# Performance work log

Measured on AMD Instinct MI355X. Metric: run time of the kernel, lower is better.

## Reference

```python
import jax, jax.numpy as jnp
import numpy as np

N_NODES = 100000
N_EDGES = 1600000
D_IN, D_HID, D_OUT = 256, 512, 48
K_STEPS = 10
ALPHA = 0.1


def setup_inputs() -> dict:
    key = jax.random.key(0)
    k_x, k_e, k_w1, k_w2 = jax.random.split(key, 4)
    x = jax.random.normal(k_x, (N_NODES, D_IN), dtype=jnp.float32)
    edge_index = jax.random.randint(k_e, (2, N_EDGES), 0, N_NODES, dtype=jnp.int64)
    # MLP params (Kaiming-ish scaling)
    W1 = jax.random.normal(k_w1, (D_IN, D_HID), dtype=jnp.float32) * (1.0 / np.sqrt(D_IN))
    b1 = jnp.zeros((D_HID,), dtype=jnp.float32)
    W2 = jax.random.normal(k_w2, (D_HID, D_OUT), dtype=jnp.float32) * (1.0 / np.sqrt(D_HID))
    b2 = jnp.zeros((D_OUT,), dtype=jnp.float32)
    return {"x": x, "edge_index": edge_index, "W1": W1, "b1": b1, "W2": W2, "b2": b2}


def reference(x, edge_index, W1, b1, W2, b2):
    N = x.shape[0]
    # --- MLP encoder ---
    h = jax.nn.relu(x @ W1 + b1) @ W2 + b2  # [N, D_OUT]

    # --- APPNP propagation (PyG defaults: add self-loops, symmetric gcn_norm) ---
    loop = jnp.arange(N, dtype=edge_index.dtype)
    src = jnp.concatenate([edge_index[0], loop])  # [E+N]
    dst = jnp.concatenate([edge_index[1], loop])
    ones = jnp.ones(src.shape[0], dtype=h.dtype)
    deg = jax.ops.segment_sum(ones, dst, num_segments=N)  # in-degree incl. self-loop
    dinv = jnp.where(deg > 0, jax.lax.rsqrt(deg), 0.0)
    norm = dinv[src] * dinv[dst]  # [E+N]

    out = h
    for _ in range(K_STEPS):
        msg = out[src] * norm[:, None]                      # gather + scale
        agg = jax.ops.segment_sum(msg, dst, num_segments=N)  # scatter-add
        out = (1.0 - ALPHA) * agg + ALPHA * h                # teleport mix
    return out
```

## Files before the change

### kernel.cpp

```cpp
#include <hip/hip_runtime.h>
#include <hip/hip_fp16.h>

constexpr int D_IN = 256, D_HID = 512, D_OUT = 48;
constexpr int HPAD = 64;
constexpr int K_STEPS = 10;

typedef __attribute__((ext_vector_type(8))) __bf16 bf16x8;
typedef __attribute__((ext_vector_type(4))) float f32x4;

__device__ __forceinline__ unsigned short f2bf(float f) {
  unsigned u = __builtin_bit_cast(unsigned, f);
  u += 0x7fffu + ((u >> 16) & 1u);
  return (unsigned short)(u >> 16);
}

__device__ __forceinline__ void gl2lds16(const unsigned short* g, unsigned short* l) {
  __builtin_amdgcn_global_load_lds(
      (const __attribute__((address_space(1))) unsigned int*)g,
      (__attribute__((address_space(3))) unsigned int*)l, 16, 0, 0);
}


__global__ void zero1_kernel(int* __restrict__ a, int N) {
  int i = blockIdx.x * 256 + threadIdx.x;
  if (i < N) a[i] = 0;
}

__global__ __launch_bounds__(256) void count_kernel(const int* __restrict__ dst,
                                                    int* __restrict__ cnt,
                                                    int* __restrict__ rank, int E) {
  int e = blockIdx.x * 256 + threadIdx.x;
  if (e >= E) return;
  int d = __builtin_nontemporal_load(dst + e);
  int r = atomicAdd(&cnt[d], 1);
  __builtin_nontemporal_store(r, rank + e);
}

__global__ void dinv_kernel(const int* __restrict__ cnt, float* __restrict__ dinv, int N) {
  int n = blockIdx.x * 256 + threadIdx.x;
  if (n < N) dinv[n] = rsqrtf((float)(cnt[n] + 1));
}

__global__ void scan1_kernel(const int* __restrict__ cnt, int* __restrict__ row_ptr,
                             int* __restrict__ bsum, int N) {
  __shared__ int sd[256];
  int tid = threadIdx.x, b = blockIdx.x;
  int i0 = b * 1024 + tid * 4;
  int v[4];
#pragma unroll
  for (int m = 0; m < 4; ++m) v[m] = (i0 + m < N) ? ((cnt[i0 + m] + 4) & ~3) : 0;
  int s = v[0] + v[1] + v[2] + v[3];
  sd[tid] = s;
  __syncthreads();
  for (int off = 1; off < 256; off <<= 1) {
    int t = (tid >= off) ? sd[tid - off] : 0;
    __syncthreads();
    sd[tid] += t;
    __syncthreads();
  }
  int run = sd[tid] - s;
#pragma unroll
  for (int m = 0; m < 4; ++m) {
    if (i0 + m < N) row_ptr[i0 + m] = run;
    run += v[m];
  }
  if (tid == 255) bsum[b] = sd[255];
}

__global__ void scan2_kernel(const int* __restrict__ bsum, int* __restrict__ bofs,
                             int* __restrict__ row_ptr, int NB, int N) {
  __shared__ int sd[128];
  int tid = threadIdx.x;
  int v = (tid < NB) ? bsum[tid] : 0;
  sd[tid] = v;
  __syncthreads();
  for (int off = 1; off < 128; off <<= 1) {
    int t = (tid >= off) ? sd[tid - off] : 0;
    __syncthreads();
    sd[tid] += t;
    __syncthreads();
  }
  if (tid < NB) bofs[tid] = sd[tid] - v;
  if (tid == 127) row_ptr[N] = sd[127];
}

__global__ void scan3_kernel(int* __restrict__ row_ptr, const int* __restrict__ bofs, int N) {
  int b = blockIdx.x;
  if (b == 0) return;
  int add = bofs[b];
  int i0 = b * 1024 + threadIdx.x * 4;
#pragma unroll
  for (int m = 0; m < 4; ++m)
    if (i0 + m < N) row_ptr[i0 + m] += add;
}

__global__ __launch_bounds__(256) void fill_kernel(
    const int* __restrict__ src, const int* __restrict__ dst,
    const int* __restrict__ row_ptr, const int* __restrict__ rank,
    int* __restrict__ edges, int E) {
  int e = blockIdx.x * 256 + threadIdx.x;
  if (e >= E) return;
  int d = __builtin_nontemporal_load(dst + e);
  int s = __builtin_nontemporal_load(src + e);
  int r = __builtin_nontemporal_load(rank + e);
  edges[row_ptr[d] + r] = s;
}

__global__ void pad_kernel(const int* __restrict__ cnt, const int* __restrict__ row_ptr,
                           int* __restrict__ edges, int N) {
  int n = blockIdx.x * 256 + threadIdx.x;
  if (n >= N) return;
  int a = row_ptr[n] + cnt[n];
  int b = row_ptr[n + 1];
  edges[a] = n;
  for (int p = a + 1; p < b; ++p) edges[p] = N;
}

__global__ void zrow_kernel(__half* __restrict__ a, __half* __restrict__ b, int N) {
  int t = threadIdx.x;
  a[(size_t)N * HPAD + t] = __float2half(0.f);
  b[(size_t)N * HPAD + t] = __float2half(0.f);
}


__global__ void convert_w1(const float* __restrict__ W1, unsigned short* __restrict__ W1F) {
  int i = blockIdx.x * 256 + threadIdx.x;
  if (i >= D_HID * D_IN) return;
  int c = i >> 8, k = i & 255;
  int ct = c >> 6, tn = (c >> 4) & 3, l15 = c & 15;
  int kb = k >> 5, q = (k >> 3) & 3, j = k & 7;
  int lane = (q << 4) | l15;
  int dst = (((ct * 4 + tn) * 8 + kb) << 9) + lane * 8 + j;
  W1F[dst] = f2bf(W1[k * D_HID + c]);
}

__global__ void convert_w2(const float* __restrict__ W2, unsigned short* __restrict__ W2F) {
  int i = blockIdx.x * 256 + threadIdx.x;
  if (i >= D_OUT * D_HID) return;
  int n = i >> 9, k = i & 511;
  int ct = k >> 6, kk = (k >> 5) & 1, q = (k >> 3) & 3, j = k & 7;
  int tn = n >> 4, l15 = n & 15;
  int lane = (q << 4) | l15;
  int dst = (((ct * 2 + kk) * 3 + tn) << 9) + lane * 8 + j;
  W2F[dst] = f2bf(W2[k * D_OUT + n]);
}


__global__ __launch_bounds__(512, 4) void encoder_kernel(
    const float* __restrict__ x, const float* __restrict__ b1,
    const float* __restrict__ b2, const float* __restrict__ dinvp,
    const unsigned short* __restrict__ W1F,
    const unsigned short* __restrict__ W2F,
    __half* __restrict__ h2, __half* __restrict__ qb, int N) {
  __shared__ unsigned short sW1[16384];
  __shared__ unsigned short sHid[8][16][72];
  __shared__ float sB1[512];
  __shared__ float sB2[64];

  int tid = threadIdx.x;
  int w = tid >> 6, lane = tid & 63;
  int q = lane >> 4, l15 = lane & 15;
  int row0 = blockIdx.x * 128 + w * 16;

  {
    const unsigned short* gsrc = W1F + (w << 9) + lane * 8;
    unsigned short* ldst = &sW1[w << 9];
#pragma unroll
    for (int i = 0; i < 4; ++i)
      gl2lds16(gsrc + (i << 12), ldst + (i << 12));
  }
  sB1[tid] = b1[tid];
  if (tid < 48) sB2[tid] = b2[tid];

  int grow = row0 + l15;
  bool rok = grow < N;
  const float* xr = x + (size_t)grow * D_IN;
  float4 xv[16];
#pragma unroll
  for (int jb = 0; jb < 8; ++jb) {
    xv[2 * jb]     = rok ? *(const float4*)(xr + jb * 32 + q * 8)
                         : make_float4(0.f, 0.f, 0.f, 0.f);
    xv[2 * jb + 1] = rok ? *(const float4*)(xr + jb * 32 + q * 8 + 4)
                         : make_float4(0.f, 0.f, 0.f, 0.f);
  }
  uint4 axu[8];
#pragma unroll
  for (int jb = 0; jb < 8; ++jb) {
    union { uint4 u; unsigned short s[8]; } uu;
    float4 v0 = xv[2 * jb], v1 = xv[2 * jb + 1];
    uu.s[0] = f2bf(v0.x); uu.s[1] = f2bf(v0.y); uu.s[2] = f2bf(v0.z); uu.s[3] = f2bf(v0.w);
    uu.s[4] = f2bf(v1.x); uu.s[5] = f2bf(v1.y); uu.s[6] = f2bf(v1.z); uu.s[7] = f2bf(v1.w);
    axu[jb] = uu.u;
  }

  f32x4 hacc[3];
#pragma unroll
  for (int t = 0; t < 3; ++t)
#pragma unroll
    for (int r = 0; r < 4; ++r) hacc[t][r] = 0.f;

  __syncthreads();

  for (int ct = 0; ct < 8; ++ct) {
    int c0 = ct * 64;
    f32x4 acc[4];
#pragma unroll
    for (int t = 0; t < 4; ++t)
#pragma unroll
      for (int r = 0; r < 4; ++r) acc[t][r] = 0.f;

    const unsigned short* sb = &sW1[lane * 8];
#pragma unroll
    for (int kb = 0; kb < 8; ++kb) {
      bf16x8 a = __builtin_bit_cast(bf16x8, axu[kb]);
      bf16x8 bq0 = *(const bf16x8*)(sb + (kb << 9));
      bf16x8 bq1 = *(const bf16x8*)(sb + (kb << 9) + 4096);
      bf16x8 bq2 = *(const bf16x8*)(sb + (kb << 9) + 8192);
      bf16x8 bq3 = *(const bf16x8*)(sb + (kb << 9) + 12288);
      acc[0] = __builtin_amdgcn_mfma_f32_16x16x32_bf16(a, bq0, acc[0], 0, 0, 0);
      acc[1] = __builtin_amdgcn_mfma_f32_16x16x32_bf16(a, bq1, acc[1], 0, 0, 0);
      acc[2] = __builtin_amdgcn_mfma_f32_16x16x32_bf16(a, bq2, acc[2], 0, 0, 0);
      acc[3] = __builtin_amdgcn_mfma_f32_16x16x32_bf16(a, bq3, acc[3], 0, 0, 0);
    }
#pragma unroll
    for (int tn = 0; tn < 4; ++tn) {
      int c = tn * 16 + l15;
      float bias = sB1[c0 + c];
#pragma unroll
      for (int rg = 0; rg < 4; ++rg) {
        float v = acc[tn][rg] + bias;
        v = v > 0.f ? v : 0.f;
        sHid[w][q * 4 + rg][c] = f2bf(v);
      }
    }
#pragma unroll
    for (int kk = 0; kk < 2; ++kk) {
      bf16x8 a0 = *(const bf16x8*)&sHid[w][l15][kk * 32 + q * 8];
      const unsigned short* w2b = W2F + (((ct * 2 + kk) * 3) << 9) + lane * 8;
#pragma unroll
      for (int tn = 0; tn < 3; ++tn) {
        bf16x8 b = *(const bf16x8*)(w2b + (tn << 9));
        hacc[tn] = __builtin_amdgcn_mfma_f32_16x16x32_bf16(a0, b, hacc[tn], 0, 0, 0);
      }
    }
    __syncthreads();
    if (ct < 7) {
      const unsigned short* gsrc = W1F + ((size_t)(ct + 1) << 14) + (w << 9) + lane * 8;
      unsigned short* ldst = &sW1[w << 9];
#pragma unroll
      for (int i = 0; i < 4; ++i)
        gl2lds16(gsrc + (i << 12), ldst + (i << 12));
      __syncthreads();
    }
  }
  float dv[4];
#pragma unroll
  for (int rg = 0; rg < 4; ++rg) {
    int gr = row0 + q * 4 + rg;
    dv[rg] = (gr < N) ? dinvp[gr] : 0.f;
  }
#pragma unroll
  for (int tn = 0; tn < 3; ++tn) {
    int c = tn * 16 + l15;
    float bias = sB2[c];
#pragma unroll
    for (int rg = 0; rg < 4; ++rg) {
      int gr = row0 + q * 4 + rg;
      if (gr < N) {
        float val = hacc[tn][rg] + bias;
        h2[(size_t)gr * HPAD + c] = __float2half(val);
        qb[(size_t)gr * HPAD + c] = __float2half(dv[rg] * val);
      }
    }
  }
#pragma unroll
  for (int rg = 0; rg < 4; ++rg) {
    int gr = row0 + q * 4 + rg;
    if (gr < N) {
      h2[(size_t)gr * HPAD + 48 + l15] = __float2half(0.f);
      qb[(size_t)gr * HPAD + 48 + l15] = __float2half(0.f);
    }
  }
}


__global__ __launch_bounds__(256) void prop_kernel(
    const __half* __restrict__ cur, const __half* __restrict__ h2,
    const float* __restrict__ dinv, const int* __restrict__ row_ptr,
    const int* __restrict__ edges, __half* __restrict__ nxt,
    float* __restrict__ outf, int N, int last) {
  int wid = (blockIdx.x * 256 + threadIdx.x) >> 6;
  int lane = threadIdx.x & 63;
  int half = lane >> 5;
  int slot = (lane >> 3) & 3;
  int s = lane & 7;
  int node = wid * 2 + half;
  bool nok = node < N;
  int p0 = 0, p1 = 0;
  if (nok) { int2 pp = *(const int2*)(row_ptr + node); p0 = pp.x; p1 = pp.y; }
  int d = p1 - p0;
  int dmax = max(d, __shfl_xor(d, 32));
  int nb = dmax >> 2;

  float acc[8];
#pragma unroll
  for (int i = 0; i < 8; ++i) acc[i] = 0.f;

  int p = p0 + slot;
  int e0 = N, e1 = N;
  if (nb > 0) e0 = edges[p];
  if (nb > 1) e1 = edges[p + 4];
  int b = 0;
  for (; b + 2 <= nb; b += 2) {
    int n0 = N, n1 = N;
    if (b + 2 < nb) n0 = edges[p + 8];
    if (b + 3 < nb) n1 = edges[p + 12];
    int i0 = (p < p1) ? e0 : N;
    int i1 = (p + 4 < p1) ? e1 : N;
    union { float4 f; __half2 h[4]; } u0, u1;
    u0.f = *(const float4*)(cur + ((size_t)i0 << 6) + s * 8);
    u1.f = *(const float4*)(cur + ((size_t)i1 << 6) + s * 8);
#pragma unroll
    for (int i = 0; i < 4; ++i) {
      float2 f0 = __half22float2(u0.h[i]);
      float2 f1 = __half22float2(u1.h[i]);
      acc[2 * i]     += f0.x + f1.x;
      acc[2 * i + 1] += f0.y + f1.y;
    }
    e0 = n0; e1 = n1; p += 8;
  }
  if (b < nb) {
    int i0 = (p < p1) ? e0 : N;
    union { float4 f; __half2 h[4]; } u0;
    u0.f = *(const float4*)(cur + ((size_t)i0 << 6) + s * 8);
#pragma unroll
    for (int i = 0; i < 4; ++i) {
      float2 f0 = __half22float2(u0.h[i]);
      acc[2 * i]     += f0.x;
      acc[2 * i + 1] += f0.y;
    }
  }
#pragma unroll
  for (int i = 0; i < 8; ++i) {
    acc[i] += __int_as_float(__builtin_amdgcn_ds_swizzle(__float_as_int(acc[i]), 0x201F));
    acc[i] += __int_as_float(__builtin_amdgcn_ds_swizzle(__float_as_int(acc[i]), 0x401F));
  }
  if ((lane & 24) != 0 || !nok) return;
  float di = dinv[node];
  size_t base = ((size_t)node << 6) + s * 8;
  union { float4 f; __half2 h[4]; } uh;
  uh.f = *(const float4*)(h2 + base);
  float outv[8];
#pragma unroll
  for (int i = 0; i < 4; ++i) {
    float2 hf = __half22float2(uh.h[i]);
    outv[2 * i]     = 0.9f * di * acc[2 * i]     + 0.1f * hf.x;
    outv[2 * i + 1] = 0.9f * di * acc[2 * i + 1] + 0.1f * hf.y;
  }
  if (last) {
    if (s < 6) {
      float* op = outf + (size_t)node * D_OUT + s * 8;
      *(float4*)op       = make_float4(outv[0], outv[1], outv[2], outv[3]);
      *(float4*)(op + 4) = make_float4(outv[4], outv[5], outv[6], outv[7]);
    }
  } else {
    union { uint4 u4; __half2 h[4]; } o;
#pragma unroll
    for (int i = 0; i < 4; ++i)
      o.h[i] = __floats2half2_rn(di * outv[2 * i], di * outv[2 * i + 1]);
    *(uint4*)(nxt + base) = o.u4;
  }
}


extern "C" void kernel_launch(void* const* d_in, const int* in_sizes, int n_in,
                              void* d_out, int out_size, void* d_ws, size_t ws_size,
                              hipStream_t stream) {
  (void)n_in; (void)out_size; (void)ws_size;
  const float* x  = (const float*)d_in[0];
  const int*   ei = (const int*)d_in[1];
  const float* W1 = (const float*)d_in[2];
  const float* b1 = (const float*)d_in[3];
  const float* W2 = (const float*)d_in[4];
  const float* b2 = (const float*)d_in[5];
  const int N = in_sizes[0] / D_IN;
  const int E = in_sizes[1] / 2;
  const int* e_src = ei;
  const int* e_dst = ei + E;

  char* ws = (char*)d_ws;
  size_t off = 0;
  auto take = [&](size_t bytes) -> char* {
    char* p = ws + off;
    off += (bytes + 511) & ~(size_t)511;
    return p;
  };
  int* cnt      = (int*)take((size_t)N * 4);
  float* dinv   = (float*)take((size_t)N * 4);
  int* row_ptr  = (int*)take((size_t)(N + 1) * 4);
  int* bsum     = (int*)take(1024);
  int* bofs     = (int*)take(1024);
  int* rank     = (int*)take((size_t)E * 4);
  int* edges    = (int*)take(((size_t)E + 4 * (size_t)N + 1024) * 4);
  unsigned short* W1F = (unsigned short*)take((size_t)D_IN * D_HID * 2);
  unsigned short* W2F = (unsigned short*)take((size_t)D_HID * D_OUT * 2);
  __half* h2    = (__half*)take((size_t)N * HPAD * 2);
  __half* bufA  = (__half*)take((size_t)(N + 1) * HPAD * 2);
  __half* bufB  = (__half*)d_out;
  float* outp   = (float*)d_out;

  int nb256 = (N + 255) / 256;
  int eb256 = (E + 255) / 256;
  int NB    = (N + 1023) / 1024;

  zero1_kernel<<<nb256, 256, 0, stream>>>(cnt, N);
  count_kernel<<<eb256, 256, 0, stream>>>(e_dst, cnt, rank, E);
  dinv_kernel<<<nb256, 256, 0, stream>>>(cnt, dinv, N);
  scan1_kernel<<<NB, 256, 0, stream>>>(cnt, row_ptr, bsum, N);
  scan2_kernel<<<1, 128, 0, stream>>>(bsum, bofs, row_ptr, NB, N);
  scan3_kernel<<<NB, 256, 0, stream>>>(row_ptr, bofs, N);
  fill_kernel<<<eb256, 256, 0, stream>>>(e_src, e_dst, row_ptr, rank, edges, E);
  pad_kernel<<<nb256, 256, 0, stream>>>(cnt, row_ptr, edges, N);
  zrow_kernel<<<1, 64, 0, stream>>>(bufA, bufB, N);

  convert_w1<<<(D_IN * D_HID + 255) / 256, 256, 0, stream>>>(W1, W1F);
  convert_w2<<<(D_HID * D_OUT + 255) / 256, 256, 0, stream>>>(W2, W2F);
  encoder_kernel<<<(N + 127) / 128, 512, 0, stream>>>(x, b1, b2, dinv, W1F, W2F,
                                                      h2, bufB, N);

  int waves = (N + 1) / 2;
  int pblocks = (waves + 3) / 4;
  const __half* src = bufB;
  __half* dst = bufA;
  for (int it = 1; it <= K_STEPS; ++it) {
    int last = (it == K_STEPS);
    prop_kernel<<<pblocks, 256, 0, stream>>>(src, h2, dinv, row_ptr, edges,
                                             dst, outp, N, last);
    src = dst;
    dst = (dst == bufA) ? bufB : bufA;
  }
}
```

Baseline: 668.9 us.

## Make encoder persistent with x prefetch overlap; unroll propagation gather by four

The encoder becomes a persistent kernel of 256 blocks that loop over 128-row strips. The next strip's x rows are prefetched into registers inside the W1-chunk loop so global loads overlap the MFMA work, and launch bounds drop to 2 waves per SIMD. Separately, the propagation kernel's neighbor gather is unrolled from 2 to 4 edge loads per iteration, with tail handling, to raise memory-level parallelism. The risks are higher register pressure and lower occupancy in the encoder, and only 256 blocks may underfill the GPU.

```diff
diff --git a/kernel.cpp b/kernel.cpp
--- a/kernel.cpp
+++ b/kernel.cpp
@@ -146,7 +146,7 @@
 }
 
 
-__global__ __launch_bounds__(512, 4) void encoder_kernel(
+__global__ __launch_bounds__(512, 2) void encoder_kernel(
     const float* __restrict__ x, const float* __restrict__ b1,
     const float* __restrict__ b2, const float* __restrict__ dinvp,
     const unsigned short* __restrict__ W1F,
@@ -160,126 +160,147 @@
   int tid = threadIdx.x;
   int w = tid >> 6, lane = tid & 63;
   int q = lane >> 4, l15 = lane & 15;
-  int row0 = blockIdx.x * 128 + w * 16;
-
-  {
-    const unsigned short* gsrc = W1F + (w << 9) + lane * 8;
+  const int nStrips = (N + 127) >> 7;
+
+  auto stageCt = [&](int c) {
+    const unsigned short* gsrc = W1F + ((size_t)c << 14) + (w << 9) + lane * 8;
     unsigned short* ldst = &sW1[w << 9];
 #pragma unroll
     for (int i = 0; i < 4; ++i)
       gl2lds16(gsrc + (i << 12), ldst + (i << 12));
-  }
+  };
+
+  int strip = blockIdx.x;
+  stageCt(0);
   sB1[tid] = b1[tid];
   if (tid < 48) sB2[tid] = b2[tid];
 
-  int grow = row0 + l15;
-  bool rok = grow < N;
-  const float* xr = x + (size_t)grow * D_IN;
   float4 xv[16];
-#pragma unroll
-  for (int jb = 0; jb < 8; ++jb) {
-    xv[2 * jb]     = rok ? *(const float4*)(xr + jb * 32 + q * 8)
-                         : make_float4(0.f, 0.f, 0.f, 0.f);
-    xv[2 * jb + 1] = rok ? *(const float4*)(xr + jb * 32 + q * 8 + 4)
-                         : make_float4(0.f, 0.f, 0.f, 0.f);
-  }
-  uint4 axu[8];
-#pragma unroll
-  for (int jb = 0; jb < 8; ++jb) {
-    union { uint4 u; unsigned short s[8]; } uu;
-    float4 v0 = xv[2 * jb], v1 = xv[2 * jb + 1];
-    uu.s[0] = f2bf(v0.x); uu.s[1] = f2bf(v0.y); uu.s[2] = f2bf(v0.z); uu.s[3] = f2bf(v0.w);
-    uu.s[4] = f2bf(v1.x); uu.s[5] = f2bf(v1.y); uu.s[6] = f2bf(v1.z); uu.s[7] = f2bf(v1.w);
-    axu[jb] = uu.u;
-  }
-
-  f32x4 hacc[3];
-#pragma unroll
-  for (int t = 0; t < 3; ++t)
-#pragma unroll
-    for (int r = 0; r < 4; ++r) hacc[t][r] = 0.f;
-
+  {
+    int grow = strip * 128 + w * 16 + l15;
+    bool rok = grow < N;
+    const float* xr = x + (size_t)grow * D_IN;
+#pragma unroll
+    for (int jb = 0; jb < 8; ++jb) {
+      xv[2 * jb]     = rok ? *(const float4*)(xr + jb * 32 + q * 8)
+                           : make_float4(0.f, 0.f, 0.f, 0.f);
+      xv[2 * jb + 1] = rok ? *(const float4*)(xr + jb * 32 + q * 8 + 4)
+                           : make_float4(0.f, 0.f, 0.f, 0.f);
+    }
+  }
   __syncthreads();
 
-  for (int ct = 0; ct < 8; ++ct) {
-    int c0 = ct * 64;
-    f32x4 acc[4];
-#pragma unroll
-    for (int t = 0; t < 4; ++t)
-#pragma unroll
-      for (int r = 0; r < 4; ++r) acc[t][r] = 0.f;
-
-    const unsigned short* sb = &sW1[lane * 8];
-#pragma unroll
-    for (int kb = 0; kb < 8; ++kb) {
-      bf16x8 a = __builtin_bit_cast(bf16x8, axu[kb]);
-      bf16x8 bq0 = *(const bf16x8*)(sb + (kb << 9));
-      bf16x8 bq1 = *(const bf16x8*)(sb + (kb << 9) + 4096);
-      bf16x8 bq2 = *(const bf16x8*)(sb + (kb << 9) + 8192);
-      bf16x8 bq3 = *(const bf16x8*)(sb + (kb << 9) + 12288);
-      acc[0] = __builtin_amdgcn_mfma_f32_16x16x32_bf16(a, bq0, acc[0], 0, 0, 0);
-      acc[1] = __builtin_amdgcn_mfma_f32_16x16x32_bf16(a, bq1, acc[1], 0, 0, 0);
-      acc[2] = __builtin_amdgcn_mfma_f32_16x16x32_bf16(a, bq2, acc[2], 0, 0, 0);
-      acc[3] = __builtin_amdgcn_mfma_f32_16x16x32_bf16(a, bq3, acc[3], 0, 0, 0);
-    }
-#pragma unroll
-    for (int tn = 0; tn < 4; ++tn) {
+  for (;;) {
+    int nxt = strip + 256;
+    bool hasNext = nxt < nStrips;
+    int ngrow = nxt * 128 + w * 16 + l15;
+    bool nok = hasNext && (ngrow < N);
+    const float* nxr = x + (size_t)ngrow * D_IN;
+
+    uint4 axu[8];
+#pragma unroll
+    for (int jb = 0; jb < 8; ++jb) {
+      union { uint4 u; unsigned short s[8]; } uu;
+      float4 v0 = xv[2 * jb], v1 = xv[2 * jb + 1];
+      uu.s[0] = f2bf(v0.x); uu.s[1] = f2bf(v0.y); uu.s[2] = f2bf(v0.z); uu.s[3] = f2bf(v0.w);
+      uu.s[4] = f2bf(v1.x); uu.s[5] = f2bf(v1.y); uu.s[6] = f2bf(v1.z); uu.s[7] = f2bf(v1.w);
+      axu[jb] = uu.u;
+    }
+
+    f32x4 hacc[3];
+#pragma unroll
+    for (int t = 0; t < 3; ++t)
+#pragma unroll
+      for (int r = 0; r < 4; ++r) hacc[t][r] = 0.f;
+
+#pragma unroll
+    for (int ct = 0; ct < 8; ++ct) {
+      int c0 = ct * 64;
+      f32x4 acc[4];
+#pragma unroll
+      for (int t = 0; t < 4; ++t)
+#pragma unroll
+        for (int r = 0; r < 4; ++r) acc[t][r] = 0.f;
+
+      const unsigned short* sb = &sW1[lane * 8];
+#pragma unroll
+      for (int kb = 0; kb < 8; ++kb) {
+        bf16x8 a = __builtin_bit_cast(bf16x8, axu[kb]);
+        bf16x8 bq0 = *(const bf16x8*)(sb + (kb << 9));
+        bf16x8 bq1 = *(const bf16x8*)(sb + (kb << 9) + 4096);
+        bf16x8 bq2 = *(const bf16x8*)(sb + (kb << 9) + 8192);
+        bf16x8 bq3 = *(const bf16x8*)(sb + (kb << 9) + 12288);
+        acc[0] = __builtin_amdgcn_mfma_f32_16x16x32_bf16(a, bq0, acc[0], 0, 0, 0);
+        acc[1] = __builtin_amdgcn_mfma_f32_16x16x32_bf16(a, bq1, acc[1], 0, 0, 0);
+        acc[2] = __builtin_amdgcn_mfma_f32_16x16x32_bf16(a, bq2, acc[2], 0, 0, 0);
+        acc[3] = __builtin_amdgcn_mfma_f32_16x16x32_bf16(a, bq3, acc[3], 0, 0, 0);
+      }
+#pragma unroll
+      for (int tn = 0; tn < 4; ++tn) {
+        int c = tn * 16 + l15;
+        float bias = sB1[c0 + c];
+#pragma unroll
+        for (int rg = 0; rg < 4; ++rg) {
+          float v = acc[tn][rg] + bias;
+          v = v > 0.f ? v : 0.f;
+          sHid[w][q * 4 + rg][c] = f2bf(v);
+        }
+      }
+#pragma unroll
+      for (int kk = 0; kk < 2; ++kk) {
+        bf16x8 a0 = *(const bf16x8*)&sHid[w][l15][kk * 32 + q * 8];
+        const unsigned short* w2b = W2F + (((ct * 2 + kk) * 3) << 9) + lane * 8;
+#pragma unroll
+        for (int tn = 0; tn < 3; ++tn) {
+          bf16x8 b = *(const bf16x8*)(w2b + (tn << 9));
+          hacc[tn] = __builtin_amdgcn_mfma_f32_16x16x32_bf16(a0, b, hacc[tn], 0, 0, 0);
+        }
+      }
+      __syncthreads();
+      if (ct < 7) stageCt(ct + 1);
+      if (hasNext) {
+        xv[2 * ct]     = nok ? *(const float4*)(nxr + ct * 32 + q * 8)
+                             : make_float4(0.f, 0.f, 0.f, 0.f);
+        xv[2 * ct + 1] = nok ? *(const float4*)(nxr + ct * 32 + q * 8 + 4)
+                             : make_float4(0.f, 0.f, 0.f, 0.f);
+      }
+      __syncthreads();
+    }
+
+    int row0 = strip * 128 + w * 16;
+    float dv[4];
+#pragma unroll
+    for (int rg = 0; rg < 4; ++rg) {
+      int gr = row0 + q * 4 + rg;
+      dv[rg] = (gr < N) ? dinvp[gr] : 0.f;
+    }
+#pragma unroll
+    for (int tn = 0; tn < 3; ++tn) {
       int c = tn * 16 + l15;
-      float bias = sB1[c0 + c];
+      float bias = sB2[c];
 #pragma unroll
       for (int rg = 0; rg < 4; ++rg) {
-        float v = acc[tn][rg] + bias;
-        v = v > 0.f ? v : 0.f;
-        sHid[w][q * 4 + rg][c] = f2bf(v);
-      }
-    }
-#pragma unroll
-    for (int kk = 0; kk < 2; ++kk) {
-      bf16x8 a0 = *(const bf16x8*)&sHid[w][l15][kk * 32 + q * 8];
-      const unsigned short* w2b = W2F + (((ct * 2 + kk) * 3) << 9) + lane * 8;
-#pragma unroll
-      for (int tn = 0; tn < 3; ++tn) {
-        bf16x8 b = *(const bf16x8*)(w2b + (tn << 9));
-        hacc[tn] = __builtin_amdgcn_mfma_f32_16x16x32_bf16(a0, b, hacc[tn], 0, 0, 0);
-      }
-    }
-    __syncthreads();
-    if (ct < 7) {
-      const unsigned short* gsrc = W1F + ((size_t)(ct + 1) << 14) + (w << 9) + lane * 8;
-      unsigned short* ldst = &sW1[w << 9];
-#pragma unroll
-      for (int i = 0; i < 4; ++i)
-        gl2lds16(gsrc + (i << 12), ldst + (i << 12));
-      __syncthreads();
-    }
-  }
-  float dv[4];
-#pragma unroll
-  for (int rg = 0; rg < 4; ++rg) {
-    int gr = row0 + q * 4 + rg;
-    dv[rg] = (gr < N) ? dinvp[gr] : 0.f;
-  }
-#pragma unroll
-  for (int tn = 0; tn < 3; ++tn) {
-    int c = tn * 16 + l15;
-    float bias = sB2[c];
+        int gr = row0 + q * 4 + rg;
+        if (gr < N) {
+          float val = hacc[tn][rg] + bias;
+          h2[(size_t)gr * HPAD + c] = __float2half(val);
+          qb[(size_t)gr * HPAD + c] = __float2half(dv[rg] * val);
+        }
+      }
+    }
 #pragma unroll
     for (int rg = 0; rg < 4; ++rg) {
       int gr = row0 + q * 4 + rg;
       if (gr < N) {
-        float val = hacc[tn][rg] + bias;
-        h2[(size_t)gr * HPAD + c] = __float2half(val);
-        qb[(size_t)gr * HPAD + c] = __float2half(dv[rg] * val);
-      }
-    }
-  }
-#pragma unroll
-  for (int rg = 0; rg < 4; ++rg) {
-    int gr = row0 + q * 4 + rg;
-    if (gr < N) {
-      h2[(size_t)gr * HPAD + 48 + l15] = __float2half(0.f);
-      qb[(size_t)gr * HPAD + 48 + l15] = __float2half(0.f);
-    }
+        h2[(size_t)gr * HPAD + 48 + l15] = __float2half(0.f);
+        qb[(size_t)gr * HPAD + 48 + l15] = __float2half(0.f);
+      }
+    }
+
+    if (!hasNext) break;
+    strip = nxt;
+    stageCt(0);
+    __syncthreads();
   }
 }
 
@@ -307,27 +328,37 @@
   for (int i = 0; i < 8; ++i) acc[i] = 0.f;
 
   int p = p0 + slot;
-  int e0 = N, e1 = N;
+  int e0 = N, e1 = N, e2 = N, e3 = N;
   if (nb > 0) e0 = edges[p];
   if (nb > 1) e1 = edges[p + 4];
+  if (nb > 2) e2 = edges[p + 8];
+  if (nb > 3) e3 = edges[p + 12];
   int b = 0;
-  for (; b + 2 <= nb; b += 2) {
-    int n0 = N, n1 = N;
-    if (b + 2 < nb) n0 = edges[p + 8];
-    if (b + 3 < nb) n1 = edges[p + 12];
-    int i0 = (p < p1) ? e0 : N;
-    int i1 = (p + 4 < p1) ? e1 : N;
-    union { float4 f; __half2 h[4]; } u0, u1;
+  for (; b + 4 <= nb; b += 4) {
+    int n0 = N, n1 = N, n2 = N, n3 = N;
+    if (b + 4 < nb) n0 = edges[p + 16];
+    if (b + 5 < nb) n1 = edges[p + 20];
+    if (b + 6 < nb) n2 = edges[p + 24];
+    if (b + 7 < nb) n3 = edges[p + 28];
+    int i0 = (p      < p1) ? e0 : N;
+    int i1 = (p + 4  < p1) ? e1 : N;
+    int i2 = (p + 8  < p1) ? e2 : N;
+    int i3 = (p + 12 < p1) ? e3 : N;
+    union { float4 f; __half2 h[4]; } u0, u1, u2, u3;
     u0.f = *(const float4*)(cur + ((size_t)i0 << 6) + s * 8);
     u1.f = *(const float4*)(cur + ((size_t)i1 << 6) + s * 8);
+    u2.f = *(const float4*)(cur + ((size_t)i2 << 6) + s * 8);
+    u3.f = *(const float4*)(cur + ((size_t)i3 << 6) + s * 8);
 #pragma unroll
     for (int i = 0; i < 4; ++i) {
       float2 f0 = __half22float2(u0.h[i]);
       float2 f1 = __half22float2(u1.h[i]);
-      acc[2 * i]     += f0.x + f1.x;
-      acc[2 * i + 1] += f0.y + f1.y;
-    }
-    e0 = n0; e1 = n1; p += 8;
+      float2 f2 = __half22float2(u2.h[i]);
+      float2 f3 = __half22float2(u3.h[i]);
+      acc[2 * i]     += (f0.x + f1.x) + (f2.x + f3.x);
+      acc[2 * i + 1] += (f0.y + f1.y) + (f2.y + f3.y);
+    }
+    e0 = n0; e1 = n1; e2 = n2; e3 = n3; p += 16;
   }
   if (b < nb) {
     int i0 = (p < p1) ? e0 : N;
@@ -338,6 +369,28 @@
       float2 f0 = __half22float2(u0.h[i]);
       acc[2 * i]     += f0.x;
       acc[2 * i + 1] += f0.y;
+    }
+  }
+  if (b + 1 < nb) {
+    int i1 = (p + 4 < p1) ? e1 : N;
+    union { float4 f; __half2 h[4]; } u1;
+    u1.f = *(const float4*)(cur + ((size_t)i1 << 6) + s * 8);
+#pragma unroll
+    for (int i = 0; i < 4; ++i) {
+      float2 f1 = __half22float2(u1.h[i]);
+      acc[2 * i]     += f1.x;
+      acc[2 * i + 1] += f1.y;
+    }
+  }
+  if (b + 2 < nb) {
+    int i2 = (p + 8 < p1) ? e2 : N;
+    union { float4 f; __half2 h[4]; } u2;
+    u2.f = *(const float4*)(cur + ((size_t)i2 << 6) + s * 8);
+#pragma unroll
+    for (int i = 0; i < 4; ++i) {
+      float2 f2 = __half22float2(u2.h[i]);
+      acc[2 * i]     += f2.x;
+      acc[2 * i + 1] += f2.y;
     }
   }
 #pragma unroll
@@ -425,8 +478,7 @@
 
   convert_w1<<<(D_IN * D_HID + 255) / 256, 256, 0, stream>>>(W1, W1F);
   convert_w2<<<(D_HID * D_OUT + 255) / 256, 256, 0, stream>>>(W2, W2F);
-  encoder_kernel<<<(N + 127) / 128, 512, 0, stream>>>(x, b1, b2, dinv, W1F, W2F,
-                                                      h2, bufB, N);
+  encoder_kernel<<<256, 512, 0, stream>>>(x, b1, b2, dinv, W1F, W2F, h2, bufB, N);
 
   int waves = (N + 1) / 2;
   int pblocks = (waves + 3) / 4;
```

After: 732.1 us. +9.4%, slower.

## Assign one wavefront per node with 8 edge slots and software-pipelined gathers

Applied to the files above, without the earlier changes.

The propagation kernel now gives each destination node a full 64-lane wavefront, with 8 edge slots of 8 lanes, instead of two nodes per wave with 4 slots each. CSR rows are padded to multiples of 8 to match, and the gather loop is rewritten with a 4-deep index prefetch and a one-ahead row load. The aim is more memory-level parallelism per node and removal of the divergent max-degree loop shared between half-waves. In exchange, rows carry more padding edges (reads of the zero row), and the wave count doubles, so more lanes sit idle for low-degree nodes.

```diff
diff --git a/kernel.cpp b/kernel.cpp
--- a/kernel.cpp
+++ b/kernel.cpp
@@ -48,7 +48,7 @@
   int i0 = b * 1024 + tid * 4;
   int v[4];
 #pragma unroll
-  for (int m = 0; m < 4; ++m) v[m] = (i0 + m < N) ? ((cnt[i0 + m] + 4) & ~3) : 0;
+  for (int m = 0; m < 4; ++m) v[m] = (i0 + m < N) ? ((cnt[i0 + m] + 8) & ~7) : 0;
   int s = v[0] + v[1] + v[2] + v[3];
   sd[tid] = s;
   __syncthreads();
@@ -291,61 +291,50 @@
     float* __restrict__ outf, int N, int last) {
   int wid = (blockIdx.x * 256 + threadIdx.x) >> 6;
   int lane = threadIdx.x & 63;
-  int half = lane >> 5;
-  int slot = (lane >> 3) & 3;
+  int slot = lane >> 3;
   int s = lane & 7;
-  int node = wid * 2 + half;
-  bool nok = node < N;
-  int p0 = 0, p1 = 0;
-  if (nok) { int2 pp = *(const int2*)(row_ptr + node); p0 = pp.x; p1 = pp.y; }
-  int d = p1 - p0;
-  int dmax = max(d, __shfl_xor(d, 32));
-  int nb = dmax >> 2;
+  int node = wid;
+  if (node >= N) return;
+  int2 pp = *(const int2*)(row_ptr + node);
+  int p = pp.x + slot;
+  int nb = (pp.y - pp.x) >> 3;
 
   float acc[8];
 #pragma unroll
   for (int i = 0; i < 8; ++i) acc[i] = 0.f;
 
-  int p = p0 + slot;
-  int e0 = N, e1 = N;
-  if (nb > 0) e0 = edges[p];
-  if (nb > 1) e1 = edges[p + 4];
-  int b = 0;
-  for (; b + 2 <= nb; b += 2) {
-    int n0 = N, n1 = N;
-    if (b + 2 < nb) n0 = edges[p + 8];
-    if (b + 3 < nb) n1 = edges[p + 12];
-    int i0 = (p < p1) ? e0 : N;
-    int i1 = (p + 4 < p1) ? e1 : N;
-    union { float4 f; __half2 h[4]; } u0, u1;
-    u0.f = *(const float4*)(cur + ((size_t)i0 << 6) + s * 8);
-    u1.f = *(const float4*)(cur + ((size_t)i1 << 6) + s * 8);
+  union F4 { float4 f; __half2 h[4]; };
+  int e1 = (1 < nb) ? edges[p + 8]  : N;
+  int e2 = (2 < nb) ? edges[p + 16] : N;
+  int e3 = (3 < nb) ? edges[p + 24] : N;
+  int e0 = edges[p];
+  F4 ucur;
+  ucur.f = *(const float4*)(cur + ((size_t)e0 << 6) + s * 8);
+
+  for (int g = 0; g < nb; ++g) {
+    int en = (g + 4 < nb) ? edges[p + ((g + 4) << 3)] : N;
+    F4 unx;
+    if (g + 1 < nb)
+      unx.f = *(const float4*)(cur + ((size_t)e1 << 6) + s * 8);
+    else
+      unx.f = make_float4(0.f, 0.f, 0.f, 0.f);
 #pragma unroll
     for (int i = 0; i < 4; ++i) {
-      float2 f0 = __half22float2(u0.h[i]);
-      float2 f1 = __half22float2(u1.h[i]);
-      acc[2 * i]     += f0.x + f1.x;
-      acc[2 * i + 1] += f0.y + f1.y;
-    }
-    e0 = n0; e1 = n1; p += 8;
-  }
-  if (b < nb) {
-    int i0 = (p < p1) ? e0 : N;
-    union { float4 f; __half2 h[4]; } u0;
-    u0.f = *(const float4*)(cur + ((size_t)i0 << 6) + s * 8);
-#pragma unroll
-    for (int i = 0; i < 4; ++i) {
-      float2 f0 = __half22float2(u0.h[i]);
-      acc[2 * i]     += f0.x;
-      acc[2 * i + 1] += f0.y;
-    }
-  }
+      float2 f = __half22float2(ucur.h[i]);
+      acc[2 * i]     += f.x;
+      acc[2 * i + 1] += f.y;
+    }
+    ucur = unx;
+    e1 = e2; e2 = e3; e3 = en;
+  }
+
 #pragma unroll
   for (int i = 0; i < 8; ++i) {
     acc[i] += __int_as_float(__builtin_amdgcn_ds_swizzle(__float_as_int(acc[i]), 0x201F));
     acc[i] += __int_as_float(__builtin_amdgcn_ds_swizzle(__float_as_int(acc[i]), 0x401F));
-  }
-  if ((lane & 24) != 0 || !nok) return;
+    acc[i] += __shfl_xor(acc[i], 32);
+  }
+  if ((lane & 56) != 0) return;
   float di = dinv[node];
   size_t base = ((size_t)node << 6) + s * 8;
   union { float4 f; __half2 h[4]; } uh;
@@ -401,7 +390,7 @@
   int* bsum     = (int*)take(1024);
   int* bofs     = (int*)take(1024);
   int* rank     = (int*)take((size_t)E * 4);
-  int* edges    = (int*)take(((size_t)E + 4 * (size_t)N + 1024) * 4);
+  int* edges    = (int*)take(((size_t)E + 8 * (size_t)N + 2048) * 4);
   unsigned short* W1F = (unsigned short*)take((size_t)D_IN * D_HID * 2);
   unsigned short* W2F = (unsigned short*)take((size_t)D_HID * D_OUT * 2);
   __half* h2    = (__half*)take((size_t)N * HPAD * 2);
@@ -428,8 +417,7 @@
   encoder_kernel<<<(N + 127) / 128, 512, 0, stream>>>(x, b1, b2, dinv, W1F, W2F,
                                                       h2, bufB, N);
 
-  int waves = (N + 1) / 2;
-  int pblocks = (waves + 3) / 4;
+  int pblocks = (N + 3) / 4;
   const __half* src = bufB;
   __half* dst = bufA;
   for (int it = 1; it <= K_STEPS; ++it) {
```

Result: slower. 744.9 us (+11.4%).
